# Kernel tuning notes

Measured on AMD Instinct MI355X. Metric: run time of the kernel, lower is better.

The kernel has to match this reference:

```python
import jax, jax.numpy as jnp
import numpy as np

D_MODEL = 256
N = 8192

def setup_inputs() -> dict:
    key = jax.random.key(0)
    k1, k2, k3, k4 = jax.random.split(key, 4)
    x = jax.random.normal(k1, (N, D_MODEL), dtype=jnp.float32)
    # nn.Linear weights: shape [out, in], applied as x @ W.T
    s = 1.0 / np.sqrt(D_MODEL)
    Wq = jax.random.normal(k2, (D_MODEL, D_MODEL), dtype=jnp.float32) * s
    Wk = jax.random.normal(k3, (D_MODEL, D_MODEL), dtype=jnp.float32) * s
    Wv = jax.random.normal(k4, (D_MODEL, D_MODEL), dtype=jnp.float32) * s
    return {"x": x, "Wq": Wq, "Wk": Wk, "Wv": Wv}

def reference(x, Wq, Wk, Wv):
    d_model = Wq.shape[0]
    Q = x @ Wq.T  # [N, d]
    K = x @ Wk.T
    V = x @ Wv.T
    scores = (Q @ K.T) / jnp.sqrt(jnp.asarray(d_model, x.dtype))  # [N, N]
    attn = jax.nn.softmax(scores, axis=-1)  # stable max-sub softmax, same math
    cntx = attn @ V  # [N, d]
    return (cntx, attn)
```

## Files before the change

### kernel.cpp

```cpp
#include <hip/hip_runtime.h>

#define D_MODEL 256
#define NSEQ    8192
#define PV_GROUPS 8

typedef _Float16 half8 __attribute__((ext_vector_type(8)));
typedef _Float16 half4 __attribute__((ext_vector_type(4)));
typedef float    f32x4 __attribute__((ext_vector_type(4)));

typedef __attribute__((address_space(1))) const void* gptr_t;
typedef __attribute__((address_space(3))) void*       lptr_t;

__device__ __forceinline__ half8 cvt8(f32x4 a, f32x4 b) {
  half8 h;
  h[0]=(_Float16)a[0]; h[1]=(_Float16)a[1]; h[2]=(_Float16)a[2]; h[3]=(_Float16)a[3];
  h[4]=(_Float16)b[0]; h[5]=(_Float16)b[1]; h[6]=(_Float16)b[2]; h[7]=(_Float16)b[3];
  return h;
}

__device__ __forceinline__ half8 load8_f32(const float* p) {
  f32x4 a = *(const f32x4*)p;
  f32x4 b = *(const f32x4*)(p + 4);
  return cvt8(a, b);
}


__global__ __launch_bounds__(64, 6) void qkv_kernel(
    const float* __restrict__ x, const float* __restrict__ Wq,
    const float* __restrict__ Wk, const float* __restrict__ Wv,
    _Float16* __restrict__ QK16, _Float16* __restrict__ VT)
{
  const int lane = threadIdx.x & 63;
  const int c    = lane & 15;
  const int quad = lane >> 4;
  const int M0   = blockIdx.x * 32;
  const int widx = blockIdx.y >> 3;
  const int nloc = (blockIdx.y & 7) * 32;
  const float* W = (widx == 0) ? Wq : (widx == 1 ? Wk : Wv);

  f32x4 acc[2][2] = {};
  for (int k0 = 0; k0 < D_MODEL; k0 += 32) {
    half8 af[2], bf[2];
#pragma unroll
    for (int mt = 0; mt < 2; ++mt)
      af[mt] = load8_f32(&x[(size_t)(M0 + mt*16 + c) * D_MODEL + k0 + quad*8]);
#pragma unroll
    for (int nt = 0; nt < 2; ++nt)
      bf[nt] = load8_f32(&W[(size_t)(nloc + nt*16 + c) * D_MODEL + k0 + quad*8]);
#pragma unroll
    for (int mt = 0; mt < 2; ++mt)
#pragma unroll
      for (int nt = 0; nt < 2; ++nt)
        acc[mt][nt] = __builtin_amdgcn_mfma_f32_16x16x32_f16(af[mt], bf[nt], acc[mt][nt], 0, 0, 0);
  }

  if (widx < 2) {
#pragma unroll
    for (int mt = 0; mt < 2; ++mt)
#pragma unroll
      for (int nt = 0; nt < 2; ++nt) {
        const int col  = widx * 256 + nloc + nt*16 + c;
        const int row0 = M0 + mt*16 + quad*4;
#pragma unroll
        for (int r = 0; r < 4; ++r)
          QK16[(size_t)(row0 + r) * 512 + col] = (_Float16)acc[mt][nt][r];
      }
  } else {
#pragma unroll
    for (int mt = 0; mt < 2; ++mt)
#pragma unroll
      for (int nt = 0; nt < 2; ++nt) {
        const int d  = nloc + nt*16 + c;
        const int m0 = M0 + mt*16 + quad*4;
        half4 h;
        h[0]=(_Float16)acc[mt][nt][0]; h[1]=(_Float16)acc[mt][nt][1];
        h[2]=(_Float16)acc[mt][nt][2]; h[3]=(_Float16)acc[mt][nt][3];
        *(half4*)&VT[(size_t)d * NSEQ + m0] = h;
      }
  }
}

template<bool P16>
__global__ __launch_bounds__(256) void score_kernel(
    const _Float16* __restrict__ QK16, void* __restrict__ Pout,
    float* __restrict__ lsum)
{
  __shared__ alignas(16) _Float16 Qs[2][8][512];
  __shared__ alignas(16) _Float16 Ks[2][8][512];
  const int tid  = threadIdx.x;
  const int lane = tid & 63;
  const int wave = tid >> 6;
  const int c    = lane & 15;
  const int quad = lane >> 4;
  const int wr   = wave >> 1;
  const int wc   = wave & 1;
  const int M0   = blockIdx.x * 128;
  const int N0   = blockIdx.y * 128;
  const int mb   = M0 + wr * 64;
  const int nb   = N0 + wc * 64;

  auto stage = [&](int buf, int k0) {
#pragma unroll
    for (int s = 0; s < 2; ++s) {
      const int t = wave * 2 + s;
      const _Float16* qsrc = &QK16[(size_t)(M0 + t*16 + (lane & 15)) * 512 + k0 + (lane >> 4) * 8];
      __builtin_amdgcn_global_load_lds((gptr_t)qsrc, (lptr_t)&Qs[buf][t][0], 16, 0, 0);
      const _Float16* ksrc = &QK16[(size_t)(N0 + t*16 + (lane & 15)) * 512 + 256 + k0 + (lane >> 4) * 8];
      __builtin_amdgcn_global_load_lds((gptr_t)ksrc, (lptr_t)&Ks[buf][t][0], 16, 0, 0);
    }
  };

  f32x4 acc[4][4] = {};
  stage(0, 0);
  __syncthreads();
  for (int it = 0; it < 8; ++it) {
    const int buf = it & 1;
    if (it < 7) stage(buf ^ 1, (it + 1) * 32);
    half8 af[4], bf[4];
#pragma unroll
    for (int mt = 0; mt < 4; ++mt)
      af[mt] = *(const half8*)&Qs[buf][wr*4 + mt][lane * 8];
#pragma unroll
    for (int nt = 0; nt < 4; ++nt)
      bf[nt] = *(const half8*)&Ks[buf][wc*4 + nt][lane * 8];
#pragma unroll
    for (int mt = 0; mt < 4; ++mt)
#pragma unroll
      for (int nt = 0; nt < 4; ++nt)
        acc[mt][nt] = __builtin_amdgcn_mfma_f32_16x16x32_f16(af[mt], bf[nt], acc[mt][nt], 0, 0, 0);
    __syncthreads();
  }

  float psum[4][4] = {};
#pragma unroll
  for (int mt = 0; mt < 4; ++mt) {
    const size_t tq = (size_t)((mb >> 4) + mt);
#pragma unroll
    for (int nt = 0; nt < 4; ++nt) {
      const size_t tj   = (size_t)((nb >> 5) + (nt >> 1));
      const size_t base = (tq * 256 + tj) * 512
                        + (size_t)(((nt*2 + (c>>3)) & 3) * 128 + quad*32 + (c & 7));
#pragma unroll
      for (int r = 0; r < 4; ++r) {
        const float p = __expf(acc[mt][nt][r] * 0.0625f);
        psum[mt][r] += p;
        if constexpr (P16) {
          ((_Float16*)Pout)[base + r*8] = (_Float16)p;
        } else {
          const size_t idx = (size_t)(mb + mt*16 + quad*4 + r) * NSEQ + nb + nt*16 + c;
          ((float*)Pout)[idx] = p;
        }
      }
    }
  }

#pragma unroll
  for (int mt = 0; mt < 4; ++mt)
#pragma unroll
    for (int r = 0; r < 4; ++r) {
      float v = psum[mt][r];
      v += __shfl_xor(v, 1);
      v += __shfl_xor(v, 2);
      v += __shfl_xor(v, 4);
      v += __shfl_xor(v, 8);
      if (c == 0) atomicAdd(&lsum[mb + mt*16 + quad*4 + r], v);
    }
}

__global__ __launch_bounds__(256) void pv_gemm_kernel(
    const _Float16* __restrict__ P16F, const _Float16* __restrict__ VT,
    float* __restrict__ cpart, int jlen)
{
  __shared__ alignas(16) _Float16 As[2][8][512];
  const int tid  = threadIdx.x;
  const int lane = tid & 63;
  const int wave = tid >> 6;
  const int c    = lane & 15;
  const int quad = lane >> 4;
  const int M0   = blockIdx.x * 64;
  const int gy   = blockIdx.y;
  const int jb   = gy * jlen;
  const int D0   = wave * 64;
  const size_t tqA = (size_t)(M0 >> 4);

  auto stage = [&](int buf, int j0) {
    const size_t tj0 = (size_t)(j0 >> 5);
#pragma unroll
    for (int s = 0; s < 2; ++s) {
      const int t = wave * 2 + s;
      const _Float16* src = &P16F[((tqA + (t >> 1)) * 256 + tj0 + (t & 1)) * 512 + lane * 8];
      __builtin_amdgcn_global_load_lds((gptr_t)src, (lptr_t)&As[buf][t][0], 16, 0, 0);
    }
  };

  f32x4 acc[4][4] = {};
  stage(0, jb);
  __syncthreads();
  const int iters = jlen >> 6;
  for (int it = 0; it < iters; ++it) {
    const int buf = it & 1;
    const int j0  = jb + it * 64;
    if (it + 1 < iters) stage(buf ^ 1, j0 + 64);

    half8 af[4][2];
#pragma unroll
    for (int mt = 0; mt < 4; ++mt)
#pragma unroll
      for (int ks = 0; ks < 2; ++ks)
        af[mt][ks] = *(const half8*)&As[buf][mt*2 + ks][lane * 8];

    half8 bf[4][2];
#pragma unroll
    for (int ks = 0; ks < 2; ++ks)
#pragma unroll
      for (int nt = 0; nt < 4; ++nt)
        bf[nt][ks] = *(const half8*)&VT[(size_t)(D0 + nt*16 + c) * NSEQ + j0 + ks*32 + quad*8];

#pragma unroll
    for (int ks = 0; ks < 2; ++ks)
#pragma unroll
      for (int mt = 0; mt < 4; ++mt)
#pragma unroll
        for (int nt = 0; nt < 4; ++nt)
          acc[mt][nt] = __builtin_amdgcn_mfma_f32_16x16x32_f16(af[mt][ks], bf[nt][ks], acc[mt][nt], 0, 0, 0);
    __syncthreads();
  }

  float* out = cpart + (size_t)gy * NSEQ * D_MODEL;
#pragma unroll
  for (int mt = 0; mt < 4; ++mt)
#pragma unroll
    for (int nt = 0; nt < 4; ++nt)
#pragma unroll
      for (int r = 0; r < 4; ++r)
        out[(size_t)(M0 + mt*16 + quad*4 + r) * D_MODEL + D0 + nt*16 + c] = acc[mt][nt][r];
}

__global__ __launch_bounds__(256, 8) void norm_kernel(
    const _Float16* __restrict__ P16F, const float* __restrict__ lsum,
    float* __restrict__ attn)
{
  const int tid = threadIdx.x;
  const int q   = tid >> 4;
  const int gl  = tid & 15;
  const int bx  = blockIdx.x;
  const int j0  = blockIdx.y * 1024;

  const float nscale = 1.0f / lsum[bx*16 + q];
  const size_t tbase = (size_t)bx * 256 + (size_t)(j0 >> 5);

#pragma unroll
  for (int it = 0; it < 8; ++it) {
    const int g = gl + it * 16;
    const half8 v = *(const half8*)&P16F[(tbase + (g >> 2)) * 512 + ((g & 3) * 16 + q) * 8];
    f32x4 w0, w1;
#pragma unroll
    for (int r = 0; r < 4; ++r) {
      w0[r] = (float)v[r]     * nscale;
      w1[r] = (float)v[r + 4] * nscale;
    }
    float* ar = attn + (size_t)(bx*16 + q) * NSEQ + j0 + g*8;
    *(f32x4*)ar       = w0;
    *(f32x4*)(ar + 4) = w1;
  }
}

__global__ __launch_bounds__(256, 8) void reduce_kernel(
    const float* __restrict__ cpart, const float* __restrict__ lsum,
    float* __restrict__ cntx, int g)
{
  const int idx4 = blockIdx.x * 256 + threadIdx.x;
  const int row  = idx4 >> 6;
  const float s  = 1.0f / lsum[row];
  f32x4 v = {};
  for (int gi = 0; gi < g; ++gi)
    v += *(const f32x4*)&cpart[(size_t)gi * NSEQ * D_MODEL + (size_t)idx4 * 4];
  *(f32x4*)&cntx[(size_t)idx4 * 4] = v * s;
}

__global__ __launch_bounds__(256) void pv_kernel_p16(
    const _Float16* __restrict__ P16F, float* __restrict__ attn,
    const float* __restrict__ lsum, const _Float16* __restrict__ VT,
    float* __restrict__ cntx)
{
  const int tid  = threadIdx.x;
  const int lane = tid & 63;
  const int wave = tid >> 6;
  const int c    = lane & 15;
  const int quad = lane >> 4;
  const int M0   = blockIdx.x * 32;
  const int jb   = blockIdx.y * (NSEQ / PV_GROUPS);
  const int je   = jb + NSEQ / PV_GROUPS;
  const int D0   = wave * 64;
  const int nq   = tid >> 3;
  const int ng   = tid & 7;

  const float nscale = 1.0f / lsum[M0 + nq];
  const size_t tqA = (size_t)(M0 >> 4);
  const size_t tqN = (size_t)((M0 + nq) >> 4);
  const int    ofsN = ((ng & 3) * 16 + ((M0 + nq) & 15)) * 8;

  f32x4 acc[2][4] = {};
  for (int j0 = jb; j0 < je; j0 += 64) {
    const size_t tj0 = (size_t)(j0 >> 5);
    half8 af[2][2];
#pragma unroll
    for (int mt = 0; mt < 2; ++mt)
#pragma unroll
      for (int ks = 0; ks < 2; ++ks)
        af[mt][ks] = *(const half8*)&P16F[((tqA + mt) * 256 + tj0 + ks) * 512 + lane * 8];
    half8 bf[4][2];
#pragma unroll
    for (int ks = 0; ks < 2; ++ks)
#pragma unroll
      for (int nt = 0; nt < 4; ++nt)
        bf[nt][ks] = *(const half8*)&VT[(size_t)(D0 + nt*16 + c) * NSEQ + j0 + ks*32 + quad*8];
    {
      const half8 v = *(const half8*)&P16F[(tqN * 256 + tj0 + (ng >> 2)) * 512 + ofsN];
      f32x4 w0, w1;
#pragma unroll
      for (int r = 0; r < 4; ++r) {
        w0[r] = (float)v[r]     * nscale;
        w1[r] = (float)v[r + 4] * nscale;
      }
      float* ar = attn + (size_t)(M0 + nq) * NSEQ + j0 + ng*8;
      *(f32x4*)ar       = w0;
      *(f32x4*)(ar + 4) = w1;
    }
#pragma unroll
    for (int ks = 0; ks < 2; ++ks)
#pragma unroll
      for (int mt = 0; mt < 2; ++mt)
#pragma unroll
        for (int nt = 0; nt < 4; ++nt)
          acc[mt][nt] = __builtin_amdgcn_mfma_f32_16x16x32_f16(af[mt][ks], bf[nt][ks], acc[mt][nt], 0, 0, 0);
  }

#pragma unroll
  for (int mt = 0; mt < 2; ++mt)
#pragma unroll
    for (int r = 0; r < 4; ++r) {
      const float s = 1.0f / lsum[M0 + mt*16 + quad*4 + r];
#pragma unroll
      for (int nt = 0; nt < 4; ++nt)
        atomicAdd(&cntx[(size_t)(M0 + mt*16 + quad*4 + r) * D_MODEL + D0 + nt*16 + c],
                  acc[mt][nt][r] * s);
    }
}

__global__ __launch_bounds__(256) void pv_kernel_f32(
    const float* __restrict__ Pin, float* __restrict__ attn,
    const float* __restrict__ lsum, const _Float16* __restrict__ VT,
    float* __restrict__ cntx)
{
  __shared__ float linv[32];
  const int tid  = threadIdx.x;
  const int lane = tid & 63;
  const int wave = tid >> 6;
  const int c    = lane & 15;
  const int quad = lane >> 4;
  const int M0   = blockIdx.x * 32;
  const int jb   = blockIdx.y * (NSEQ / PV_GROUPS);
  const int je   = jb + NSEQ / PV_GROUPS;
  const int D0   = wave * 64;
  const int nr   = tid >> 3;
  const int ncol = (tid & 7) * 8;

  if (tid < 32) linv[tid] = 1.0f / lsum[M0 + tid];
  __syncthreads();
  const float nscale = linv[nr];

  f32x4 acc[2][4] = {};
  for (int j0 = jb; j0 < je; j0 += 64) {
    const float* pr = Pin + (size_t)(M0 + nr) * NSEQ + j0 + ncol;
    f32x4 np0 = *(const f32x4*)pr;
    f32x4 np1 = *(const f32x4*)(pr + 4);

    half8 af[2][2], bf[4][2];
#pragma unroll
    for (int h = 0; h < 2; ++h) {
#pragma unroll
      for (int mt = 0; mt < 2; ++mt) {
        const float* pa = Pin + (size_t)(M0 + mt*16 + c) * NSEQ + j0 + h*32 + quad*8;
        af[mt][h] = cvt8(*(const f32x4*)pa, *(const f32x4*)(pa + 4));
      }
#pragma unroll
      for (int nt = 0; nt < 4; ++nt)
        bf[nt][h] = *(const half8*)&VT[(size_t)(D0 + nt*16 + c) * NSEQ + j0 + h*32 + quad*8];
    }

    __syncthreads();

    float* ar = attn + (size_t)(M0 + nr) * NSEQ + j0 + ncol;
    *(f32x4*)ar       = np0 * nscale;
    *(f32x4*)(ar + 4) = np1 * nscale;

#pragma unroll
    for (int h = 0; h < 2; ++h)
#pragma unroll
      for (int mt = 0; mt < 2; ++mt)
#pragma unroll
        for (int nt = 0; nt < 4; ++nt)
          acc[mt][nt] = __builtin_amdgcn_mfma_f32_16x16x32_f16(af[mt][h], bf[nt][h], acc[mt][nt], 0, 0, 0);
  }

#pragma unroll
  for (int mt = 0; mt < 2; ++mt)
#pragma unroll
    for (int r = 0; r < 4; ++r) {
      const float s = linv[mt*16 + quad*4 + r];
#pragma unroll
      for (int nt = 0; nt < 4; ++nt)
        atomicAdd(&cntx[(size_t)(M0 + mt*16 + quad*4 + r) * D_MODEL + D0 + nt*16 + c],
                  acc[mt][nt][r] * s);
    }
}

extern "C" void kernel_launch(void* const* d_in, const int* in_sizes, int n_in,
                              void* d_out, int out_size, void* d_ws, size_t ws_size,
                              hipStream_t stream)
{
  const float* x  = (const float*)d_in[0];
  const float* Wq = (const float*)d_in[1];
  const float* Wk = (const float*)d_in[2];
  const float* Wv = (const float*)d_in[3];

  float* cntx = (float*)d_out;
  float* attn = cntx + (size_t)NSEQ * D_MODEL;

  _Float16* QK16 = (_Float16*)d_ws;
  _Float16* VT   = QK16 + (size_t)NSEQ * 512;
  float*    lsum = (float*)(VT + (size_t)D_MODEL * NSEQ);
  _Float16* P16F = (_Float16*)(lsum + NSEQ);
  float*    cpart = (float*)(P16F + (size_t)NSEQ * NSEQ);

  const size_t base_bytes = (size_t)NSEQ*512*2 + (size_t)D_MODEL*NSEQ*2 + (size_t)NSEQ*4;
  const size_t p16_bytes  = (size_t)NSEQ * NSEQ * 2;
  const size_t part_bytes = (size_t)NSEQ * D_MODEL * 4;

  int g = 0;
  for (int gt = 8; gt >= 2; gt >>= 1)
    if (ws_size >= base_bytes + p16_bytes + (size_t)gt * part_bytes) { g = gt; break; }
  const bool big_ws = ws_size >= base_bytes + p16_bytes;

  hipMemsetAsync(lsum, 0, sizeof(float) * NSEQ, stream);

  qkv_kernel<<<dim3(256, 24), 64, 0, stream>>>(x, Wq, Wk, Wv, QK16, VT);

  if (g >= 2) {
    score_kernel<true><<<dim3(64, 64), 256, 0, stream>>>(QK16, (void*)P16F, lsum);
    pv_gemm_kernel<<<dim3(128, g), 256, 0, stream>>>(P16F, VT, cpart, NSEQ / g);
    norm_kernel<<<dim3(512, 8), 256, 0, stream>>>(P16F, lsum, attn);
    reduce_kernel<<<dim3(NSEQ * D_MODEL / 1024), 256, 0, stream>>>(cpart, lsum, cntx, g);
  } else if (big_ws) {
    hipMemsetAsync(cntx, 0, sizeof(float) * (size_t)NSEQ * D_MODEL, stream);
    score_kernel<true><<<dim3(64, 64), 256, 0, stream>>>(QK16, (void*)P16F, lsum);
    pv_kernel_p16<<<dim3(NSEQ/32, PV_GROUPS), 256, 0, stream>>>(P16F, attn, lsum, VT, cntx);
  } else {
    hipMemsetAsync(cntx, 0, sizeof(float) * (size_t)NSEQ * D_MODEL, stream);
    score_kernel<false><<<dim3(64, 64), 256, 0, stream>>>(QK16, (void*)attn, lsum);
    pv_kernel_f32<<<dim3(NSEQ/32, PV_GROUPS), 256, 0, stream>>>(attn, attn, lsum, VT, cntx);
  }
}
```

Before: 557.8 us.

## Fuse attention normalization into PV GEMM using staged LDS tiles

Removes the separate norm kernel that re-read the fp16 probability matrix from global memory. The PV GEMM kernel now reads each staged LDS tile, scales it by the inverse row sum and writes normalized fp32 attention rows while it runs the MFMA accumulation. This saves a full 128 MB fp16 re-read and one kernel launch. In exchange the GEMM kernel takes on heavy global store traffic (256 MB fp32), which may slow its MFMA loop or lower occupancy.

```diff
diff --git a/kernel.cpp b/kernel.cpp
--- a/kernel.cpp
+++ b/kernel.cpp
@@ -169,9 +169,11 @@
 
 __global__ __launch_bounds__(256) void pv_gemm_kernel(
     const _Float16* __restrict__ P16F, const _Float16* __restrict__ VT,
+    const float* __restrict__ lsum, float* __restrict__ attn,
     float* __restrict__ cpart, int jlen)
 {
   __shared__ alignas(16) _Float16 As[2][8][512];
+  __shared__ float linv[64];
   const int tid  = threadIdx.x;
   const int lane = tid & 63;
   const int wave = tid >> 6;
@@ -182,6 +184,8 @@
   const int jb   = gy * jlen;
   const int D0   = wave * 64;
   const size_t tqA = (size_t)(M0 >> 4);
+  const int nq   = tid >> 2;
+  const int g0   = tid & 3;
 
   auto stage = [&](int buf, int j0) {
     const size_t tj0 = (size_t)(j0 >> 5);
@@ -193,9 +197,13 @@
     }
   };
 
+  if (tid < 64) linv[tid] = 1.0f / lsum[M0 + tid];
+
   f32x4 acc[4][4] = {};
   stage(0, jb);
   __syncthreads();
+  const float nscale = linv[nq];
+
   const int iters = jlen >> 6;
   for (int it = 0; it < iters; ++it) {
     const int buf = it & 1;
@@ -217,6 +225,22 @@
         bf[nt][ks] = *(const half8*)&VT[(size_t)(D0 + nt*16 + c) * NSEQ + j0 + ks*32 + quad*8];
 
 #pragma unroll
+    for (int h = 0; h < 2; ++h) {
+      const int g = g0 + h*4;
+      const int t = ((nq >> 4) << 1) + (g >> 2);
+      const half8 v = *(const half8*)&As[buf][t][((g & 3) * 16 + (nq & 15)) * 8];
+      f32x4 w0, w1;
+#pragma unroll
+      for (int r = 0; r < 4; ++r) {
+        w0[r] = (float)v[r]     * nscale;
+        w1[r] = (float)v[r + 4] * nscale;
+      }
+      float* ar = attn + (size_t)(M0 + nq) * NSEQ + j0 + g*8;
+      *(f32x4*)ar       = w0;
+      *(f32x4*)(ar + 4) = w1;
+    }
+
+#pragma unroll
     for (int ks = 0; ks < 2; ++ks)
 #pragma unroll
       for (int mt = 0; mt < 4; ++mt)
@@ -234,35 +258,6 @@
 #pragma unroll
       for (int r = 0; r < 4; ++r)
         out[(size_t)(M0 + mt*16 + quad*4 + r) * D_MODEL + D0 + nt*16 + c] = acc[mt][nt][r];
-}
-
-__global__ __launch_bounds__(256, 8) void norm_kernel(
-    const _Float16* __restrict__ P16F, const float* __restrict__ lsum,
-    float* __restrict__ attn)
-{
-  const int tid = threadIdx.x;
-  const int q   = tid >> 4;
-  const int gl  = tid & 15;
-  const int bx  = blockIdx.x;
-  const int j0  = blockIdx.y * 1024;
-
-  const float nscale = 1.0f / lsum[bx*16 + q];
-  const size_t tbase = (size_t)bx * 256 + (size_t)(j0 >> 5);
-
-#pragma unroll
-  for (int it = 0; it < 8; ++it) {
-    const int g = gl + it * 16;
-    const half8 v = *(const half8*)&P16F[(tbase + (g >> 2)) * 512 + ((g & 3) * 16 + q) * 8];
-    f32x4 w0, w1;
-#pragma unroll
-    for (int r = 0; r < 4; ++r) {
-      w0[r] = (float)v[r]     * nscale;
-      w1[r] = (float)v[r + 4] * nscale;
-    }
-    float* ar = attn + (size_t)(bx*16 + q) * NSEQ + j0 + g*8;
-    *(f32x4*)ar       = w0;
-    *(f32x4*)(ar + 4) = w1;
-  }
 }
 
 __global__ __launch_bounds__(256, 8) void reduce_kernel(
@@ -449,8 +444,7 @@
 
   if (g >= 2) {
     score_kernel<true><<<dim3(64, 64), 256, 0, stream>>>(QK16, (void*)P16F, lsum);
-    pv_gemm_kernel<<<dim3(128, g), 256, 0, stream>>>(P16F, VT, cpart, NSEQ / g);
-    norm_kernel<<<dim3(512, 8), 256, 0, stream>>>(P16F, lsum, attn);
+    pv_gemm_kernel<<<dim3(128, g), 256, 0, stream>>>(P16F, VT, lsum, attn, cpart, NSEQ / g);
     reduce_kernel<<<dim3(NSEQ * D_MODEL / 1024), 256, 0, stream>>>(cpart, lsum, cntx, g);
   } else if (big_ws) {
     hipMemsetAsync(cntx, 0, sizeof(float) * (size_t)NSEQ * D_MODEL, stream);
```

Result: faster. 546.3 us (-2.1%).
